# Kernel optimization log

Measured on AMD Instinct MI355X. Metric: run time of the kernel, lower is better.

The kernel has to match this reference:

```python
import jax, jax.numpy as jnp
import numpy as np

B, S = 32, 128
VIDEO_SIZE, TITLE_SIZE = 768, 768
NUM_TAG, NUM_VOCAB, HIDDEN = 10000, 21128, 256


def setup_inputs() -> dict:
    key = jax.random.key(0)
    ks = jax.random.split(key, 10)
    video_feature = jax.random.normal(ks[0], (B, VIDEO_SIZE), dtype=jnp.float32)
    title_feature = jax.random.normal(ks[1], (B, S, TITLE_SIZE), dtype=jnp.float32)
    label_tag = jax.random.uniform(ks[2], (B, NUM_TAG), dtype=jnp.float32)
    label_mlm = jax.random.randint(ks[3], (B, S), 0, NUM_VOCAB, dtype=jnp.int64)
    Wt = jax.random.normal(ks[4], (NUM_TAG, VIDEO_SIZE), dtype=jnp.float32) * 0.02
    bt = jnp.zeros((NUM_TAG,), dtype=jnp.float32)
    Wm = jax.random.normal(ks[5], (NUM_VOCAB, TITLE_SIZE), dtype=jnp.float32) * 0.02
    bm = jnp.zeros((NUM_VOCAB,), dtype=jnp.float32)
    Wh = jax.random.normal(ks[6], (HIDDEN, VIDEO_SIZE + TITLE_SIZE), dtype=jnp.float32) * 0.02
    bh = jnp.zeros((HIDDEN,), dtype=jnp.float32)
    return {
        "video_feature": video_feature,
        "title_feature": title_feature,
        "label_tag": label_tag,
        "label_mlm": label_mlm,
        "Wt": Wt, "bt": bt, "Wm": Wm, "bm": bm, "Wh": Wh, "bh": bh,
    }


def reference(video_feature, title_feature, label_tag, label_mlm, Wt, bt, Wm, bm, Wh, bh):
    # tag head + BCEWithLogits (mean reduction), numerically stable form
    pred_tag = video_feature @ Wt.T + bt                       # [B, NUM_TAG]
    loss_tag = jnp.mean(
        jnp.maximum(pred_tag, 0.0) - pred_tag * label_tag
        + jnp.log1p(jnp.exp(-jnp.abs(pred_tag)))
    )
    pred_tag_sig = jax.nn.sigmoid(pred_tag)

    # mlm head: per-token vocab logits, masked CE summed over nonzero labels
    logits = jnp.einsum('bsd,vd->bsv', title_feature, Wm) + bm  # [B, S, V]
    lse = jax.nn.logsumexp(logits, axis=-1)                     # [B, S]
    gold = jnp.take_along_axis(logits, label_mlm[..., None], axis=-1)[..., 0]
    ce = lse - gold                                             # per-token NLL
    mask = (label_mlm != 0)
    loss_mlm = jnp.sum(jnp.where(mask, ce, 0.0))

    # fused embedding head + L2 normalize (torch eps 1e-12)
    feature = jnp.concatenate([video_feature, title_feature[:, 0]], axis=1)
    embedding = feature @ Wh.T + bh                             # [B, HIDDEN]
    norm = jnp.linalg.norm(embedding, axis=1, keepdims=True)
    normed_embedding = embedding / jnp.maximum(norm, 1e-12)

    return (pred_tag_sig, normed_embedding, loss_tag, loss_mlm)
```

## Files before the change

### kernel.cpp

```cpp
#include <hip/hip_runtime.h>
#include <hip/hip_bf16.h>
#include <math.h>

typedef short bf16x8 __attribute__((ext_vector_type(8)));
typedef float f32x4 __attribute__((ext_vector_type(4)));

#define KDIM 768
#define NTAG 10000
#define NVOC 21128
#define HID 256
#define NTOK 4096
#define NCHUNK 24
#define CHUNK 881
#define NTILE 56
#define TILEB 12288
#define M0 4.0f
#define WMSCALE 16.0f
#define INVSCALE 0.0625f
#define LOG2E 1.44269504f

#define WS_A     0ull
#define WS_AVID  3145728ull
#define WS_PSUM  3194880ull
#define WS_GOLD  3588096ull
#define WS_TAGL  3604480ull
#define WS_WM8   3604544ull
#define WS_NEED  (WS_WM8 + 16515072ull + 65536ull)

#define OUT_EMB  320000
#define OUT_LTAG 328192
#define OUT_LMLM 328193

#define TAG_BLKS 313
#define GOLD_BLKS 1024
#define EMB_BLKS 32

typedef const __attribute__((address_space(1))) unsigned int glds_g;
typedef __attribute__((address_space(3))) unsigned int glds_l;

static __device__ __forceinline__ unsigned short f2bf(float f) {
  unsigned u = __builtin_bit_cast(unsigned, f);
  u = u + 0x7FFFu + ((u >> 16) & 1u);
  return (unsigned short)(u >> 16);
}

static __device__ __forceinline__ int pk4_fp8(float4 v, float scale) {
  int w = __builtin_amdgcn_cvt_pk_fp8_f32(v.x * scale, v.y * scale, 0, false);
  w = __builtin_amdgcn_cvt_pk_fp8_f32(v.z * scale, v.w * scale, w, true);
  return w;
}

__global__ __launch_bounds__(256) void k_conv(
    const float* __restrict__ title, const float* __restrict__ video,
    char* __restrict__ A8, unsigned short* __restrict__ Avid,
    float* __restrict__ tagSum) {
  const int nT = 393216;
  const int nV = 3072;
  int i = blockIdx.x * 256 + threadIdx.x;
  if (i == 0) tagSum[0] = 0.f;
  if (i < nT) {
    float4 v0 = ((const float4*)title)[i * 2];
    float4 v1 = ((const float4*)title)[i * 2 + 1];
    int2 o = {pk4_fp8(v0, 1.f), pk4_fp8(v1, 1.f)};
    *(int2*)(A8 + (size_t)i * 8) = o;
  } else if (i < nT + nV) {
    int j = i - nT;
    float4 v0 = ((const float4*)video)[j * 2];
    float4 v1 = ((const float4*)video)[j * 2 + 1];
    bf16x8 o;
    o[0] = (short)f2bf(v0.x); o[1] = (short)f2bf(v0.y);
    o[2] = (short)f2bf(v0.z); o[3] = (short)f2bf(v0.w);
    o[4] = (short)f2bf(v1.x); o[5] = (short)f2bf(v1.y);
    o[6] = (short)f2bf(v1.z); o[7] = (short)f2bf(v1.w);
    *(bf16x8*)(Avid + (size_t)j * 8) = o;
  }
}

__global__ __launch_bounds__(256) void k_convwm(
    const float* __restrict__ Wm, char* __restrict__ Wm8) {
  const int blk = blockIdx.x, tid = threadIdx.x;
  const int chunk = blk / NTILE, tile = blk % NTILE;
  const int n0 = chunk * CHUNK + tile * 16;
  const int nend = min(chunk * CHUNK + CHUNK, NVOC);
  char* dst = Wm8 + (size_t)blk * TILEB;
  #pragma unroll
  for (int j = 0; j < 6; ++j) {
    int piece = j * 256 + tid;
    int kk = piece >> 6, g = (piece >> 4) & 3, nl = piece & 15;
    int n = n0 + nl;
    int2 o = {0, 0};
    if (n < nend) {
      const float* wp = Wm + (size_t)n * KDIM + kk * 32 + g * 8;
      float4 f0 = ((const float4*)wp)[0], f1 = ((const float4*)wp)[1];
      o.x = pk4_fp8(f0, WMSCALE);
      o.y = pk4_fp8(f1, WMSCALE);
    }
    *(int2*)(dst + piece * 8) = o;
  }
}

template<bool WM8>
__global__ __launch_bounds__(256)
__attribute__((amdgpu_waves_per_eu(3, 3)))
void k_mlm(
    const char* __restrict__ A8,
    const float* __restrict__ Wm,
    const char* __restrict__ Wm8,
    const float* __restrict__ bm,
    float* __restrict__ psum) {
  __shared__ __align__(1024) char Bsm[2][TILEB];
  __shared__ float biasS[NTILE * 16];
  const int tid = threadIdx.x;
  const int lane = tid & 63, g = lane >> 4, col = lane & 15;
  const int wave = tid >> 6;
  const int chunk = blockIdx.x % NCHUNK, mt = blockIdx.x / NCHUNK;
  const int nbeg = chunk * CHUNK;
  const int nend = min(nbeg + CHUNK, NVOC);

  for (int i = tid; i < NTILE * 16; i += 256) {
    int n = nbeg + i;
    biasS[i] = (n < nend) ? (bm[n] - M0) * LOG2E : -1e30f;
  }

  const int arow0 = mt * 128 + wave * 32;
  long a0[24], a1[24];
  #pragma unroll
  for (int kk = 0; kk < 24; ++kk) {
    a0[kk] = *(const long*)(A8 + (size_t)(arow0 + col) * KDIM + kk * 32 + g * 8);
    a1[kk] = *(const long*)(A8 + (size_t)(arow0 + 16 + col) * KDIM + kk * 32 + g * 8);
  }

  float s[8];
  #pragma unroll
  for (int i = 0; i < 8; ++i) s[i] = 0.f;

  const int off0 = col * 8 + g * 128;
  const float kinv = INVSCALE * LOG2E;

  auto COMPUTE = [&](int t) {
    const char* B = &Bsm[t & 1][0] + off0;
    f32x4 acc0 = {0.f, 0.f, 0.f, 0.f}, acc1 = {0.f, 0.f, 0.f, 0.f};
    #pragma unroll
    for (int kk = 0; kk < 24; ++kk) {
      long b = *(const long*)(B + kk * 512);
      acc0 = __builtin_amdgcn_mfma_f32_16x16x32_fp8_fp8(a0[kk], b, acc0, 0, 0, 0);
      acc1 = __builtin_amdgcn_mfma_f32_16x16x32_fp8_fp8(a1[kk], b, acc1, 0, 0, 0);
    }
    const float bias2 = biasS[t * 16 + col];
    #pragma unroll
    for (int rr = 0; rr < 4; ++rr) {
      s[rr]     += exp2f(fmaf(acc0[rr], kinv, bias2));
      s[rr + 4] += exp2f(fmaf(acc1[rr], kinv, bias2));
    }
  };

  if constexpr (WM8) {
    const char* cbase = Wm8 + (size_t)chunk * NTILE * TILEB;
    auto STAGE = [&](int buf, int tt) {
      const char* src = cbase + (size_t)tt * TILEB + (wave * 64 + lane) * 16;
      char* dst = &Bsm[buf][0] + wave * 1024;
      #pragma unroll
      for (int j = 0; j < 3; ++j) {
        __builtin_amdgcn_global_load_lds((glds_g*)(src + j * 4096),
                                         (glds_l*)(dst + j * 4096), 16, 0, 0);
      }
    };
    STAGE(0, 0);
    asm volatile("s_waitcnt lgkmcnt(0)" ::: "memory");
    __builtin_amdgcn_s_barrier();
    for (int t = 0; t < NTILE; ++t) {
      int tn = (t + 1 < NTILE) ? t + 1 : 0;
      STAGE((t + 1) & 1, tn);
      asm volatile("s_waitcnt vmcnt(3)" ::: "memory");
      __builtin_amdgcn_s_barrier();
      __builtin_amdgcn_sched_barrier(0);
      __builtin_amdgcn_s_setprio(1);
      COMPUTE(t);
      __builtin_amdgcn_s_setprio(0);
      __builtin_amdgcn_sched_barrier(0);
      __builtin_amdgcn_s_barrier();
    }
  } else {
    __syncthreads();
    for (int t = 0; t < NTILE; ++t) {
      #pragma unroll
      for (int j = 0; j < 3; ++j) {
        int sg = j * 256 + tid;
        int kk = sg >> 5, gg = (sg >> 3) & 3, nl0 = (sg & 7) * 2;
        int n_a = nbeg + t * 16 + nl0, n_b = n_a + 1;
        int4 o = {0, 0, 0, 0};
        if (n_a < nend) {
          const float* wp = Wm + (size_t)n_a * KDIM + kk * 32 + gg * 8;
          o.x = pk4_fp8(((const float4*)wp)[0], WMSCALE);
          o.y = pk4_fp8(((const float4*)wp)[1], WMSCALE);
        }
        if (n_b < nend) {
          const float* wp = Wm + (size_t)n_b * KDIM + kk * 32 + gg * 8;
          o.z = pk4_fp8(((const float4*)wp)[0], WMSCALE);
          o.w = pk4_fp8(((const float4*)wp)[1], WMSCALE);
        }
        *(int4*)(&Bsm[0][0] + sg * 16) = o;
      }
      __syncthreads();
      COMPUTE(t);
      __syncthreads();
    }
  }

  #pragma unroll
  for (int i = 0; i < 8; ++i) {
    float v = s[i];
    v += __shfl_xor(v, 1);
    v += __shfl_xor(v, 2);
    v += __shfl_xor(v, 4);
    v += __shfl_xor(v, 8);
    s[i] = v;
  }
  if (col == 0) {
    #pragma unroll
    for (int mblk = 0; mblk < 2; ++mblk)
      #pragma unroll
      for (int rr = 0; rr < 4; ++rr) {
        int tok = arow0 + mblk * 16 + g * 4 + rr;
        psum[tok * NCHUNK + chunk] = s[mblk * 4 + rr];
      }
  }
}

__global__ __launch_bounds__(256) void k_tail(
    const unsigned short* __restrict__ Avid,
    const float* __restrict__ Wt, const float* __restrict__ bt,
    const float* __restrict__ ylab,
    const float* __restrict__ title, const int* __restrict__ lab,
    const float* __restrict__ Wm, const float* __restrict__ bm,
    const float* __restrict__ video,
    const float* __restrict__ Wh, const float* __restrict__ bh,
    float* __restrict__ out_sig, float* __restrict__ tagSum,
    float* __restrict__ gold, float* __restrict__ out_emb) {
  __shared__ __align__(1024) char smem[49664];
  const int bid = blockIdx.x, tid = threadIdx.x;
  const int wave = tid >> 6, lane = tid & 63, g = lane >> 4, col = lane & 15;

  if (bid < TAG_BLKS) {
    unsigned short* Bt = (unsigned short*)smem;
    float* wsum = (float*)(smem + 49152);
    #pragma unroll
    for (int j = 0; j < 12; ++j) {
      int sg = j * 256 + tid;
      int tt = (j >= 6) ? 1 : 0;
      int sgl = sg - tt * 1536;
      int kk = sgl >> 6, c = (sgl & 63) >> 2, gg = sgl & 3;
      int n = (bid * 2 + tt) * 16 + c;
      bf16x8 o = {};
      if (n < NTAG) {
        const float* wp = Wt + (size_t)n * KDIM + kk * 32 + gg * 8;
        float4 f0 = ((const float4*)wp)[0], f1 = ((const float4*)wp)[1];
        o[0] = (short)f2bf(f0.x); o[1] = (short)f2bf(f0.y);
        o[2] = (short)f2bf(f0.z); o[3] = (short)f2bf(f0.w);
        o[4] = (short)f2bf(f1.x); o[5] = (short)f2bf(f1.y);
        o[6] = (short)f2bf(f1.z); o[7] = (short)f2bf(f1.w);
      }
      *(bf16x8*)((char*)Bt + sg * 16) = o;
    }
    __syncthreads();

    const int ntile = bid * 2 + (wave >> 1), mhalf = wave & 1;
    float lacc = 0.f;
    if (ntile < 625) {
      bf16x8 a[24];
      #pragma unroll
      for (int kk = 0; kk < 24; ++kk)
        a[kk] = *(const bf16x8*)(Avid + (size_t)(mhalf * 16 + col) * KDIM + kk * 32 + g * 8);
      const char* Bb = (const char*)Bt + (wave >> 1) * 24576 + col * 64 + g * 16;
      f32x4 acc = {0.f, 0.f, 0.f, 0.f};
      #pragma unroll
      for (int kk = 0; kk < 24; ++kk) {
        bf16x8 b = *(const bf16x8*)(Bb + kk * 1024);
        acc = __builtin_amdgcn_mfma_f32_16x16x32_bf16(a[kk], b, acc, 0, 0, 0);
      }
      const int nc = ntile * 16 + col;
      if (nc < NTAG) {
        const float bias = bt[nc];
        #pragma unroll
        for (int rr = 0; rr < 4; ++rr) {
          int brow = mhalf * 16 + g * 4 + rr;
          float x = acc[rr] + bias;
          out_sig[(size_t)brow * NTAG + nc] = 1.f / (1.f + __expf(-x));
          float y = ylab[(size_t)brow * NTAG + nc];
          lacc += fmaxf(x, 0.f) - x * y + log1pf(__expf(-fabsf(x)));
        }
      }
    }
    #pragma unroll
    for (int m = 32; m; m >>= 1) lacc += __shfl_xor(lacc, m);
    if (lane == 0) wsum[wave] = lacc;
    __syncthreads();
    if (tid == 0) atomicAdd(tagSum, wsum[0] + wsum[1] + wsum[2] + wsum[3]);

  } else if (bid < TAG_BLKS + GOLD_BLKS) {
    int tok = (bid - TAG_BLKS) * 4 + wave;
    int l = lab[tok];
    float acc = 0.f;
    #pragma unroll
    for (int j = 0; j < 12; ++j) {
      int k = j * 64 + lane;
      acc += title[(size_t)tok * KDIM + k] * Wm[(size_t)l * KDIM + k];
    }
    #pragma unroll
    for (int m = 32; m; m >>= 1) acc += __shfl_xor(acc, m);
    if (lane == 0) gold[tok] = acc + bm[l];

  } else {
    float* feat = (float*)smem;
    float* red = (float*)(smem + 49152);
    const int b = bid - TAG_BLKS - GOLD_BLKS;
    #pragma unroll
    for (int j = 0; j < 6; ++j) {
      int k = j * 256 + tid;
      feat[k] = (k < KDIM) ? video[(size_t)b * KDIM + k]
                           : title[(size_t)b * 128 * KDIM + (k - KDIM)];
    }
    __syncthreads();
    float acc = bh[tid];
    #pragma unroll 8
    for (int k = 0; k < 1536; k += 4) {
      float4 w = *(const float4*)(Wh + (size_t)tid * 1536 + k);
      acc += w.x * feat[k] + w.y * feat[k + 1] + w.z * feat[k + 2] + w.w * feat[k + 3];
    }
    float ss = acc * acc;
    #pragma unroll
    for (int m = 32; m; m >>= 1) ss += __shfl_xor(ss, m);
    if (lane == 0) red[wave] = ss;
    __syncthreads();
    float nrm = sqrtf(red[0] + red[1] + red[2] + red[3]);
    float scale = 1.f / fmaxf(nrm, 1e-12f);
    out_emb[(size_t)b * HID + tid] = acc * scale;
  }
}

__global__ __launch_bounds__(256) void k_final(
    const float* __restrict__ psum, const float* __restrict__ gold,
    const int* __restrict__ lab, const float* __restrict__ tagSum,
    float* __restrict__ out) {
  __shared__ float red[4];
  const int tid = threadIdx.x, wave = tid >> 6, lane = tid & 63;
  if (tid == 0) out[OUT_LTAG] = tagSum[0] / 320000.f;

  float lm = 0.f;
  for (int tok = tid; tok < NTOK; tok += 256) {
    float S = 0.f;
    #pragma unroll
    for (int c = 0; c < NCHUNK; ++c) S += psum[tok * NCHUNK + c];
    float lse = M0 + logf(S);
    if (lab[tok] != 0) lm += lse - gold[tok];
  }
  #pragma unroll
  for (int m = 32; m; m >>= 1) lm += __shfl_xor(lm, m);
  if (lane == 0) red[wave] = lm;
  __syncthreads();
  if (tid == 0) out[OUT_LMLM] = red[0] + red[1] + red[2] + red[3];
}

extern "C" void kernel_launch(void* const* d_in, const int* in_sizes, int n_in,
                              void* d_out, int out_size, void* d_ws, size_t ws_size,
                              hipStream_t stream) {
  const float* video = (const float*)d_in[0];
  const float* title = (const float*)d_in[1];
  const float* ylab  = (const float*)d_in[2];
  const int*   lab   = (const int*)d_in[3];
  const float* Wt = (const float*)d_in[4];
  const float* bt = (const float*)d_in[5];
  const float* Wm = (const float*)d_in[6];
  const float* bm = (const float*)d_in[7];
  const float* Wh = (const float*)d_in[8];
  const float* bh = (const float*)d_in[9];
  float* out = (float*)d_out;
  char* ws = (char*)d_ws;

  char* wsA8   = ws + WS_A;
  unsigned short* wsAvid = (unsigned short*)(ws + WS_AVID);
  float* wsPsum = (float*)(ws + WS_PSUM);
  float* wsGold = (float*)(ws + WS_GOLD);
  float* wsTagl = (float*)(ws + WS_TAGL);
  char* wsWm8  = ws + WS_WM8;

  const bool useWm8 = ws_size >= WS_NEED;

  k_conv<<<1549, 256, 0, stream>>>(title, video, wsA8, wsAvid, wsTagl);
  if (useWm8) {
    k_convwm<<<NCHUNK * NTILE, 256, 0, stream>>>(Wm, wsWm8);
    k_mlm<true><<<768, 256, 0, stream>>>(wsA8, Wm, wsWm8, bm, wsPsum);
  } else {
    k_mlm<false><<<768, 256, 0, stream>>>(wsA8, Wm, wsWm8, bm, wsPsum);
  }
  k_tail<<<TAG_BLKS + GOLD_BLKS + EMB_BLKS, 256, 0, stream>>>(
      wsAvid, Wt, bt, ylab, title, lab, Wm, bm, video, Wh, bh,
      out, wsTagl, wsGold, out + OUT_EMB);
  k_final<<<1, 256, 0, stream>>>(wsPsum, wsGold, lab, wsTagl, out);
}
```

Measured before the change: 194.2 us.

## Merge conversion kernels and MLM with tail into fewer launches, widen vocab tile

```diff
diff --git a/kernel.cpp b/kernel.cpp
--- a/kernel.cpp
+++ b/kernel.cpp
@@ -12,8 +12,8 @@
 #define NTOK 4096
 #define NCHUNK 24
 #define CHUNK 881
-#define NTILE 56
-#define TILEB 12288
+#define NTILE 28
+#define TILEB 24576
 #define M0 4.0f
 #define WMSCALE 16.0f
 #define INVSCALE 0.0625f
@@ -31,9 +31,12 @@
 #define OUT_LTAG 328192
 #define OUT_LMLM 328193
 
+#define MLM_BLKS 768
 #define TAG_BLKS 313
 #define GOLD_BLKS 1024
 #define EMB_BLKS 32
+#define CONV_BLKS 1548
+#define WMCV_BLKS (NCHUNK*NTILE)
 
 typedef const __attribute__((address_space(1))) unsigned int glds_g;
 typedef __attribute__((address_space(3))) unsigned int glds_l;
@@ -52,196 +55,203 @@
 
 __global__ __launch_bounds__(256) void k_conv(
     const float* __restrict__ title, const float* __restrict__ video,
+    const float* __restrict__ Wm,
     char* __restrict__ A8, unsigned short* __restrict__ Avid,
-    float* __restrict__ tagSum) {
-  const int nT = 393216;
-  const int nV = 3072;
-  int i = blockIdx.x * 256 + threadIdx.x;
-  if (i == 0) tagSum[0] = 0.f;
-  if (i < nT) {
-    float4 v0 = ((const float4*)title)[i * 2];
-    float4 v1 = ((const float4*)title)[i * 2 + 1];
-    int2 o = {pk4_fp8(v0, 1.f), pk4_fp8(v1, 1.f)};
-    *(int2*)(A8 + (size_t)i * 8) = o;
-  } else if (i < nT + nV) {
-    int j = i - nT;
-    float4 v0 = ((const float4*)video)[j * 2];
-    float4 v1 = ((const float4*)video)[j * 2 + 1];
-    bf16x8 o;
-    o[0] = (short)f2bf(v0.x); o[1] = (short)f2bf(v0.y);
-    o[2] = (short)f2bf(v0.z); o[3] = (short)f2bf(v0.w);
-    o[4] = (short)f2bf(v1.x); o[5] = (short)f2bf(v1.y);
-    o[6] = (short)f2bf(v1.z); o[7] = (short)f2bf(v1.w);
-    *(bf16x8*)(Avid + (size_t)j * 8) = o;
-  }
-}
-
-__global__ __launch_bounds__(256) void k_convwm(
-    const float* __restrict__ Wm, char* __restrict__ Wm8) {
-  const int blk = blockIdx.x, tid = threadIdx.x;
-  const int chunk = blk / NTILE, tile = blk % NTILE;
-  const int n0 = chunk * CHUNK + tile * 16;
-  const int nend = min(chunk * CHUNK + CHUNK, NVOC);
-  char* dst = Wm8 + (size_t)blk * TILEB;
-  #pragma unroll
-  for (int j = 0; j < 6; ++j) {
-    int piece = j * 256 + tid;
-    int kk = piece >> 6, g = (piece >> 4) & 3, nl = piece & 15;
-    int n = n0 + nl;
-    int2 o = {0, 0};
-    if (n < nend) {
-      const float* wp = Wm + (size_t)n * KDIM + kk * 32 + g * 8;
-      float4 f0 = ((const float4*)wp)[0], f1 = ((const float4*)wp)[1];
-      o.x = pk4_fp8(f0, WMSCALE);
-      o.y = pk4_fp8(f1, WMSCALE);
-    }
-    *(int2*)(dst + piece * 8) = o;
+    char* __restrict__ Wm8, float* __restrict__ tagSum) {
+  __shared__ __align__(1024) char tsm[TILEB];
+  const int bid = blockIdx.x, tid = threadIdx.x;
+  if (bid < CONV_BLKS) {
+    const int nT = 393216;
+    int i = bid * 256 + tid;
+    if (i == 0) tagSum[0] = 0.f;
+    if (i < nT) {
+      float4 v0 = ((const float4*)title)[i * 2];
+      float4 v1 = ((const float4*)title)[i * 2 + 1];
+      int2 o = {pk4_fp8(v0, 1.f), pk4_fp8(v1, 1.f)};
+      *(int2*)(A8 + (size_t)i * 8) = o;
+    } else {
+      int j = i - nT;
+      float4 v0 = ((const float4*)video)[j * 2];
+      float4 v1 = ((const float4*)video)[j * 2 + 1];
+      bf16x8 o;
+      o[0] = (short)f2bf(v0.x); o[1] = (short)f2bf(v0.y);
+      o[2] = (short)f2bf(v0.z); o[3] = (short)f2bf(v0.w);
+      o[4] = (short)f2bf(v1.x); o[5] = (short)f2bf(v1.y);
+      o[6] = (short)f2bf(v1.z); o[7] = (short)f2bf(v1.w);
+      *(bf16x8*)(Avid + (size_t)j * 8) = o;
+    }
+  } else {
+    const int wblk = bid - CONV_BLKS;
+    const int chunk = wblk / NTILE, tile = wblk % NTILE;
+    const int n0 = chunk * CHUNK + tile * 32;
+    const int nend = min(chunk * CHUNK + CHUNK, NVOC);
+    #pragma unroll
+    for (int j = 0; j < 12; ++j) {
+      int p = j * 256 + tid;
+      int r = p / 96, q = p % 96;
+      int n = n0 + r;
+      int2 o = {0, 0};
+      if (n < nend) {
+        const float* wp = Wm + (size_t)n * KDIM + q * 8;
+        o.x = pk4_fp8(((const float4*)wp)[0], WMSCALE);
+        o.y = pk4_fp8(((const float4*)wp)[1], WMSCALE);
+      }
+      *(int2*)(tsm + (q >> 2) * 1024 + (q & 3) * 256 + r * 8) = o;
+    }
+    __syncthreads();
+    char* dst = Wm8 + (size_t)wblk * TILEB;
+    #pragma unroll
+    for (int j = 0; j < 6; ++j) {
+      int idx = j * 256 + tid;
+      *(int4*)(dst + idx * 16) = *(const int4*)(tsm + idx * 16);
+    }
   }
 }
 
 template<bool WM8>
 __global__ __launch_bounds__(256)
 __attribute__((amdgpu_waves_per_eu(3, 3)))
-void k_mlm(
+void k_main(
     const char* __restrict__ A8,
     const float* __restrict__ Wm,
     const char* __restrict__ Wm8,
     const float* __restrict__ bm,
-    float* __restrict__ psum) {
-  __shared__ __align__(1024) char Bsm[2][TILEB];
-  __shared__ float biasS[NTILE * 16];
-  const int tid = threadIdx.x;
-  const int lane = tid & 63, g = lane >> 4, col = lane & 15;
-  const int wave = tid >> 6;
-  const int chunk = blockIdx.x % NCHUNK, mt = blockIdx.x / NCHUNK;
-  const int nbeg = chunk * CHUNK;
-  const int nend = min(nbeg + CHUNK, NVOC);
-
-  for (int i = tid; i < NTILE * 16; i += 256) {
-    int n = nbeg + i;
-    biasS[i] = (n < nend) ? (bm[n] - M0) * LOG2E : -1e30f;
-  }
-
-  const int arow0 = mt * 128 + wave * 32;
-  long a0[24], a1[24];
-  #pragma unroll
-  for (int kk = 0; kk < 24; ++kk) {
-    a0[kk] = *(const long*)(A8 + (size_t)(arow0 + col) * KDIM + kk * 32 + g * 8);
-    a1[kk] = *(const long*)(A8 + (size_t)(arow0 + 16 + col) * KDIM + kk * 32 + g * 8);
-  }
-
-  float s[8];
-  #pragma unroll
-  for (int i = 0; i < 8; ++i) s[i] = 0.f;
-
-  const int off0 = col * 8 + g * 128;
-  const float kinv = INVSCALE * LOG2E;
-
-  auto COMPUTE = [&](int t) {
-    const char* B = &Bsm[t & 1][0] + off0;
-    f32x4 acc0 = {0.f, 0.f, 0.f, 0.f}, acc1 = {0.f, 0.f, 0.f, 0.f};
-    #pragma unroll
-    for (int kk = 0; kk < 24; ++kk) {
-      long b = *(const long*)(B + kk * 512);
-      acc0 = __builtin_amdgcn_mfma_f32_16x16x32_fp8_fp8(a0[kk], b, acc0, 0, 0, 0);
-      acc1 = __builtin_amdgcn_mfma_f32_16x16x32_fp8_fp8(a1[kk], b, acc1, 0, 0, 0);
-    }
-    const float bias2 = biasS[t * 16 + col];
-    #pragma unroll
-    for (int rr = 0; rr < 4; ++rr) {
-      s[rr]     += exp2f(fmaf(acc0[rr], kinv, bias2));
-      s[rr + 4] += exp2f(fmaf(acc1[rr], kinv, bias2));
-    }
-  };
-
-  if constexpr (WM8) {
-    const char* cbase = Wm8 + (size_t)chunk * NTILE * TILEB;
-    auto STAGE = [&](int buf, int tt) {
-      const char* src = cbase + (size_t)tt * TILEB + (wave * 64 + lane) * 16;
-      char* dst = &Bsm[buf][0] + wave * 1024;
-      #pragma unroll
-      for (int j = 0; j < 3; ++j) {
-        __builtin_amdgcn_global_load_lds((glds_g*)(src + j * 4096),
-                                         (glds_l*)(dst + j * 4096), 16, 0, 0);
-      }
-    };
-    STAGE(0, 0);
-    asm volatile("s_waitcnt lgkmcnt(0)" ::: "memory");
-    __builtin_amdgcn_s_barrier();
-    for (int t = 0; t < NTILE; ++t) {
-      int tn = (t + 1 < NTILE) ? t + 1 : 0;
-      STAGE((t + 1) & 1, tn);
-      asm volatile("s_waitcnt vmcnt(3)" ::: "memory");
-      __builtin_amdgcn_s_barrier();
-      __builtin_amdgcn_sched_barrier(0);
-      __builtin_amdgcn_s_setprio(1);
-      COMPUTE(t);
-      __builtin_amdgcn_s_setprio(0);
-      __builtin_amdgcn_sched_barrier(0);
-      __builtin_amdgcn_s_barrier();
-    }
-  } else {
-    __syncthreads();
-    for (int t = 0; t < NTILE; ++t) {
-      #pragma unroll
-      for (int j = 0; j < 3; ++j) {
-        int sg = j * 256 + tid;
-        int kk = sg >> 5, gg = (sg >> 3) & 3, nl0 = (sg & 7) * 2;
-        int n_a = nbeg + t * 16 + nl0, n_b = n_a + 1;
-        int4 o = {0, 0, 0, 0};
-        if (n_a < nend) {
-          const float* wp = Wm + (size_t)n_a * KDIM + kk * 32 + gg * 8;
-          o.x = pk4_fp8(((const float4*)wp)[0], WMSCALE);
-          o.y = pk4_fp8(((const float4*)wp)[1], WMSCALE);
-        }
-        if (n_b < nend) {
-          const float* wp = Wm + (size_t)n_b * KDIM + kk * 32 + gg * 8;
-          o.z = pk4_fp8(((const float4*)wp)[0], WMSCALE);
-          o.w = pk4_fp8(((const float4*)wp)[1], WMSCALE);
-        }
-        *(int4*)(&Bsm[0][0] + sg * 16) = o;
-      }
-      __syncthreads();
-      COMPUTE(t);
-      __syncthreads();
-    }
-  }
-
-  #pragma unroll
-  for (int i = 0; i < 8; ++i) {
-    float v = s[i];
-    v += __shfl_xor(v, 1);
-    v += __shfl_xor(v, 2);
-    v += __shfl_xor(v, 4);
-    v += __shfl_xor(v, 8);
-    s[i] = v;
-  }
-  if (col == 0) {
-    #pragma unroll
-    for (int mblk = 0; mblk < 2; ++mblk)
-      #pragma unroll
-      for (int rr = 0; rr < 4; ++rr) {
-        int tok = arow0 + mblk * 16 + g * 4 + rr;
-        psum[tok * NCHUNK + chunk] = s[mblk * 4 + rr];
-      }
-  }
-}
-
-__global__ __launch_bounds__(256) void k_tail(
+    float* __restrict__ psum,
     const unsigned short* __restrict__ Avid,
     const float* __restrict__ Wt, const float* __restrict__ bt,
     const float* __restrict__ ylab,
     const float* __restrict__ title, const int* __restrict__ lab,
-    const float* __restrict__ Wm, const float* __restrict__ bm,
     const float* __restrict__ video,
     const float* __restrict__ Wh, const float* __restrict__ bh,
     float* __restrict__ out_sig, float* __restrict__ tagSum,
     float* __restrict__ gold, float* __restrict__ out_emb) {
-  __shared__ __align__(1024) char smem[49664];
+  __shared__ __align__(1024) char smem[2 * TILEB + 3584];
   const int bid = blockIdx.x, tid = threadIdx.x;
   const int wave = tid >> 6, lane = tid & 63, g = lane >> 4, col = lane & 15;
 
-  if (bid < TAG_BLKS) {
+  if (bid < MLM_BLKS) {
+    char (*Bsm)[TILEB] = (char(*)[TILEB])smem;
+    float* biasS = (float*)(smem + 2 * TILEB);
+    const int chunk = bid % NCHUNK, mt = bid / NCHUNK;
+    const int nbeg = chunk * CHUNK;
+    const int nend = min(nbeg + CHUNK, NVOC);
+
+    for (int i = tid; i < NTILE * 32; i += 256) {
+      int n = nbeg + i;
+      biasS[i] = (n < nend) ? (bm[n] - M0) * LOG2E : -1e30f;
+    }
+
+    const int arow0 = mt * 128 + wave * 32;
+    long a0[24], a1[24];
+    #pragma unroll
+    for (int kk = 0; kk < 24; ++kk) {
+      a0[kk] = *(const long*)(A8 + (size_t)(arow0 + col) * KDIM + kk * 32 + g * 8);
+      a1[kk] = *(const long*)(A8 + (size_t)(arow0 + 16 + col) * KDIM + kk * 32 + g * 8);
+    }
+
+    float s[8];
+    #pragma unroll
+    for (int i = 0; i < 8; ++i) s[i] = 0.f;
+
+    const int off0 = col * 8 + g * 256;
+    const float kinv = INVSCALE * LOG2E;
+
+    auto COMPUTE = [&](int t) {
+      const char* B = &Bsm[t & 1][0] + off0;
+      f32x4 acc00 = {0.f,0.f,0.f,0.f}, acc10 = {0.f,0.f,0.f,0.f};
+      f32x4 acc01 = {0.f,0.f,0.f,0.f}, acc11 = {0.f,0.f,0.f,0.f};
+      #pragma unroll
+      for (int kk = 0; kk < 24; ++kk) {
+        long b0 = *(const long*)(B + kk * 1024);
+        long b1 = *(const long*)(B + kk * 1024 + 128);
+        acc00 = __builtin_amdgcn_mfma_f32_16x16x32_fp8_fp8(a0[kk], b0, acc00, 0, 0, 0);
+        acc10 = __builtin_amdgcn_mfma_f32_16x16x32_fp8_fp8(a1[kk], b0, acc10, 0, 0, 0);
+        acc01 = __builtin_amdgcn_mfma_f32_16x16x32_fp8_fp8(a0[kk], b1, acc01, 0, 0, 0);
+        acc11 = __builtin_amdgcn_mfma_f32_16x16x32_fp8_fp8(a1[kk], b1, acc11, 0, 0, 0);
+      }
+      const float b20 = biasS[t * 32 + col];
+      const float b21 = biasS[t * 32 + 16 + col];
+      #pragma unroll
+      for (int rr = 0; rr < 4; ++rr) {
+        s[rr]     += exp2f(fmaf(acc00[rr], kinv, b20)) + exp2f(fmaf(acc01[rr], kinv, b21));
+        s[rr + 4] += exp2f(fmaf(acc10[rr], kinv, b20)) + exp2f(fmaf(acc11[rr], kinv, b21));
+      }
+    };
+
+    if constexpr (WM8) {
+      const char* cbase = Wm8 + (size_t)chunk * NTILE * TILEB;
+      auto STAGE = [&](int buf, int tt) {
+        const char* src = cbase + (size_t)tt * TILEB + wave * 1024 + lane * 16;
+        char* dst = &Bsm[buf][0] + wave * 1024;
+        #pragma unroll
+        for (int j = 0; j < 6; ++j) {
+          __builtin_amdgcn_global_load_lds((glds_g*)(src + j * 4096),
+                                           (glds_l*)(dst + j * 4096), 16, 0, 0);
+        }
+      };
+      STAGE(0, 0);
+      asm volatile("s_waitcnt lgkmcnt(0)" ::: "memory");
+      __builtin_amdgcn_s_barrier();
+      for (int t = 0; t < NTILE; ++t) {
+        int tn = (t + 1 < NTILE) ? t + 1 : 0;
+        STAGE((t + 1) & 1, tn);
+        asm volatile("s_waitcnt vmcnt(6)" ::: "memory");
+        __builtin_amdgcn_s_barrier();
+        __builtin_amdgcn_sched_barrier(0);
+        __builtin_amdgcn_s_setprio(1);
+        COMPUTE(t);
+        __builtin_amdgcn_s_setprio(0);
+        __builtin_amdgcn_sched_barrier(0);
+        __builtin_amdgcn_s_barrier();
+      }
+    } else {
+      __syncthreads();
+      for (int t = 0; t < NTILE; ++t) {
+        #pragma unroll
+        for (int j = 0; j < 6; ++j) {
+          int sg = j * 256 + tid;
+          int kk = sg >> 6, gg = (sg >> 4) & 3, nl0 = (sg & 15) * 2;
+          int n_a = nbeg + t * 32 + nl0, n_b = n_a + 1;
+          int4 o = {0, 0, 0, 0};
+          if (n_a < nend) {
+            const float* wp = Wm + (size_t)n_a * KDIM + kk * 32 + gg * 8;
+            o.x = pk4_fp8(((const float4*)wp)[0], WMSCALE);
+            o.y = pk4_fp8(((const float4*)wp)[1], WMSCALE);
+          }
+          if (n_b < nend) {
+            const float* wp = Wm + (size_t)n_b * KDIM + kk * 32 + gg * 8;
+            o.z = pk4_fp8(((const float4*)wp)[0], WMSCALE);
+            o.w = pk4_fp8(((const float4*)wp)[1], WMSCALE);
+          }
+          *(int4*)(&Bsm[0][0] + sg * 16) = o;
+        }
+        __syncthreads();
+        COMPUTE(t);
+        __syncthreads();
+      }
+    }
+
+    #pragma unroll
+    for (int i = 0; i < 8; ++i) {
+      float v = s[i];
+      v += __shfl_xor(v, 1);
+      v += __shfl_xor(v, 2);
+      v += __shfl_xor(v, 4);
+      v += __shfl_xor(v, 8);
+      s[i] = v;
+    }
+    if (col == 0) {
+      #pragma unroll
+      for (int mblk = 0; mblk < 2; ++mblk)
+        #pragma unroll
+        for (int rr = 0; rr < 4; ++rr) {
+          int tok = arow0 + mblk * 16 + g * 4 + rr;
+          psum[tok * NCHUNK + chunk] = s[mblk * 4 + rr];
+        }
+    }
+
+  } else if (bid < MLM_BLKS + TAG_BLKS) {
+    const int tb = bid - MLM_BLKS;
     unsigned short* Bt = (unsigned short*)smem;
     float* wsum = (float*)(smem + 49152);
     #pragma unroll
@@ -250,7 +260,7 @@
       int tt = (j >= 6) ? 1 : 0;
       int sgl = sg - tt * 1536;
       int kk = sgl >> 6, c = (sgl & 63) >> 2, gg = sgl & 3;
-      int n = (bid * 2 + tt) * 16 + c;
+      int n = (tb * 2 + tt) * 16 + c;
       bf16x8 o = {};
       if (n < NTAG) {
         const float* wp = Wt + (size_t)n * KDIM + kk * 32 + gg * 8;
@@ -264,7 +274,7 @@
     }
     __syncthreads();
 
-    const int ntile = bid * 2 + (wave >> 1), mhalf = wave & 1;
+    const int ntile = tb * 2 + (wave >> 1), mhalf = wave & 1;
     float lacc = 0.f;
     if (ntile < 625) {
       bf16x8 a[24];
@@ -297,8 +307,8 @@
     __syncthreads();
     if (tid == 0) atomicAdd(tagSum, wsum[0] + wsum[1] + wsum[2] + wsum[3]);
 
-  } else if (bid < TAG_BLKS + GOLD_BLKS) {
-    int tok = (bid - TAG_BLKS) * 4 + wave;
+  } else if (bid < MLM_BLKS + TAG_BLKS + GOLD_BLKS) {
+    int tok = (bid - MLM_BLKS - TAG_BLKS) * 4 + wave;
     int l = lab[tok];
     float acc = 0.f;
     #pragma unroll
@@ -313,7 +323,7 @@
   } else {
     float* feat = (float*)smem;
     float* red = (float*)(smem + 49152);
-    const int b = bid - TAG_BLKS - GOLD_BLKS;
+    const int b = bid - MLM_BLKS - TAG_BLKS - GOLD_BLKS;
     #pragma unroll
     for (int j = 0; j < 6; ++j) {
       int k = j * 256 + tid;
@@ -385,16 +395,17 @@
   char* wsWm8  = ws + WS_WM8;
 
   const bool useWm8 = ws_size >= WS_NEED;
-
-  k_conv<<<1549, 256, 0, stream>>>(title, video, wsA8, wsAvid, wsTagl);
-  if (useWm8) {
-    k_convwm<<<NCHUNK * NTILE, 256, 0, stream>>>(Wm, wsWm8);
-    k_mlm<true><<<768, 256, 0, stream>>>(wsA8, Wm, wsWm8, bm, wsPsum);
-  } else {
-    k_mlm<false><<<768, 256, 0, stream>>>(wsA8, Wm, wsWm8, bm, wsPsum);
-  }
-  k_tail<<<TAG_BLKS + GOLD_BLKS + EMB_BLKS, 256, 0, stream>>>(
-      wsAvid, Wt, bt, ylab, title, lab, Wm, bm, video, Wh, bh,
-      out, wsTagl, wsGold, out + OUT_EMB);
+  const int mainGrid = MLM_BLKS + TAG_BLKS + GOLD_BLKS + EMB_BLKS;
+
+  k_conv<<<CONV_BLKS + WMCV_BLKS, 256, 0, stream>>>(
+      title, video, Wm, wsA8, wsAvid, wsWm8, wsTagl);
+  if (useWm8)
+    k_main<true><<<mainGrid, 256, 0, stream>>>(
+        wsA8, Wm, wsWm8, bm, wsPsum, wsAvid, Wt, bt, ylab, title, lab,
+        video, Wh, bh, out, wsTagl, wsGold, out + OUT_EMB);
+  else
+    k_main<false><<<mainGrid, 256, 0, stream>>>(
+        wsA8, Wm, wsWm8, bm, wsPsum, wsAvid, Wt, bt, ylab, title, lab,
+        video, Wh, bh, out, wsTagl, wsGold, out + OUT_EMB);
   k_final<<<1, 256, 0, stream>>>(wsPsum, wsGold, lab, wsTagl, out);
 }
```

Result: faster. 163.4 us (-15.9%).
